# Optimization experiments

Hardware: AMD Instinct MI355X
Metric: run time of the kernel (lower is better)

Reference implementation:

```python
import jax, jax.numpy as jnp
import numpy as np

P = 16          # patch size
NH = 12         # num heads
DH = 64         # head dim
C = 768         # embed dim
DEPTH = 12
HID = 3072      # mlp hidden = 4*C
EPS = 1e-6


def _ln(x, g, b):
    m = x.mean(-1, keepdims=True)
    v = ((x - m) ** 2).mean(-1, keepdims=True)
    return (x - m) / jnp.sqrt(v + EPS) * g + b


def _rope_tables(seq_len, dim):
    inv_freq = 1.0 / (10000.0 ** (jnp.arange(0, dim, 2, dtype=jnp.float32) / dim))
    freqs = jnp.arange(seq_len, dtype=jnp.float32)[:, None] * inv_freq[None, :]  # [S, dim/2]
    emb = jnp.concatenate([freqs, freqs], axis=-1)  # [S, dim] (concat layout, as in source)
    return jnp.cos(emb), jnp.sin(emb)


def _apply_rope(q, k, cos, sin):
    def rot(t):  # interleaved rotate-half, exactly as torch source
        t1, t2 = t[..., ::2], t[..., 1::2]
        return jnp.stack([-t2, t1], axis=-1).reshape(t.shape)
    return q * cos + rot(q) * sin, k * cos + rot(k) * sin


def setup_inputs() -> dict:
    key = jax.random.key(0)
    ks = jax.random.split(key, 16)
    w = lambda k, shp: (jax.random.normal(k, shp, dtype=jnp.float32) * 0.02)
    inp = {
        "x": jax.random.normal(ks[0], (4, 6, 320, 320), dtype=jnp.float32),
        "conv_w": w(ks[1], (C, 3, P, P)),
        "conv_b": jnp.zeros((C,), jnp.float32),
        "ln1_g": jnp.ones((DEPTH, C), jnp.float32),
        "ln1_b": jnp.zeros((DEPTH, C), jnp.float32),
        "qkv_w": w(ks[2], (DEPTH, C, 3 * C)),
        "qkv_b": jnp.zeros((DEPTH, 3 * C), jnp.float32),
        "proj_w": w(ks[3], (DEPTH, C, C)),
        "proj_b": jnp.zeros((DEPTH, C), jnp.float32),
        "ln2_g": jnp.ones((DEPTH, C), jnp.float32),
        "ln2_b": jnp.zeros((DEPTH, C), jnp.float32),
        "fc1_w": w(ks[4], (DEPTH, C, HID)),
        "fc1_b": jnp.zeros((DEPTH, HID), jnp.float32),
        "fc2_w": w(ks[5], (DEPTH, HID, C)),
        "fc2_b": jnp.zeros((DEPTH, C), jnp.float32),
        "lnf_g": jnp.ones((C,), jnp.float32),
        "lnf_b": jnp.zeros((C,), jnp.float32),
    }
    return inp


def reference(x, conv_w, conv_b, ln1_g, ln1_b, qkv_w, qkv_b, proj_w, proj_b,
              ln2_g, ln2_b, fc1_w, fc1_b, fc2_w, fc2_b, lnf_g, lnf_b):
    B = x.shape[0]

    def embed(img):  # [B,3,H,W] -> [B, (H/P)*(W/P), C]
        y = jax.lax.conv_general_dilated(
            img, conv_w, window_strides=(P, P), padding="VALID",
            dimension_numbers=("NCHW", "OIHW", "NCHW")) + conv_b[None, :, None, None]
        b, c, hg, wg = y.shape
        return y.reshape(b, c, hg * wg).transpose(0, 2, 1)

    t = jnp.concatenate([embed(x[:, :3]), embed(x[:, 3:])], axis=1)  # [B,S,C], S=2*400=800
    S = t.shape[1]
    cos, sin = _rope_tables(S, DH)
    cos, sin = cos[None, None], sin[None, None]  # [1,1,S,DH]
    scale = DH ** -0.5

    def block(h, p):
        l1g, l1b, qw, qb, pw, pb, l2g, l2b, f1w, f1b, f2w, f2b = p
        y = _ln(h, l1g, l1b)
        qkv = (y @ qw + qb).reshape(B, S, 3, NH, DH).transpose(2, 0, 3, 1, 4)
        q, k, v = qkv[0], qkv[1], qkv[2]  # [B,NH,S,DH]
        q, k = _apply_rope(q, k, cos, sin)
        a = jax.nn.softmax(jnp.einsum("bhsd,bhtd->bhst", q, k) * scale, axis=-1)
        o = jnp.einsum("bhst,bhtd->bhsd", a, v).transpose(0, 2, 1, 3).reshape(B, S, C)
        h = h + (o @ pw + pb)
        y = _ln(h, l2g, l2b)
        h = h + (jax.nn.gelu(y @ f1w + f1b, approximate=False) @ f2w + f2b)
        return h, None

    params = (ln1_g, ln1_b, qkv_w, qkv_b, proj_w, proj_b,
              ln2_g, ln2_b, fc1_w, fc1_b, fc2_w, fc2_b)
    t, _ = jax.lax.scan(block, t, params)
    return _ln(t, lnf_g, lnf_b)
```

## Files before the change

kernel.cpp:

```cpp
#include <hip/hip_runtime.h>
#include <hip/hip_bf16.h>
#include <math.h>

#define S_LEN   800
#define SP_LEN  896
#define C_DIM   768
#define NHEAD   12
#define DHEAD   64
#define HID_DIM 3072
#define BATCH   4
#define NTOK    (BATCH * S_LEN)
#define DEPTH_N 12

using bf16x8 = __attribute__((ext_vector_type(8))) short;
using f32x4  = __attribute__((ext_vector_type(4))) float;

__device__ inline short f2bf(float x) {
    unsigned u = __builtin_bit_cast(unsigned, x);
    u += 0x7fff + ((u >> 16) & 1);
    return (short)(u >> 16);
}
__device__ inline float bf2f(short x) {
    unsigned u = ((unsigned)(unsigned short)x) << 16;
    return __builtin_bit_cast(float, u);
}

typedef const __attribute__((address_space(1))) void* gas_ptr;
typedef __attribute__((address_space(3))) void* las_ptr;
__device__ inline void async_copy16(const void* g, void* l) {
    __builtin_amdgcn_global_load_lds((gas_ptr)g, (las_ptr)l, 16, 0, 0);
}

__global__ __launch_bounds__(256)
void transpose_convert_kernel(const float* __restrict__ W, short* __restrict__ Wt,
                              int K, int N) {
    __shared__ float tile[32][33];
    int k0 = blockIdx.y * 32, n0 = blockIdx.x * 32;
    int tx = threadIdx.x & 31, ty = threadIdx.x >> 5;
#pragma unroll
    for (int i = ty; i < 32; i += 8)
        tile[i][tx] = W[(size_t)(k0 + i) * N + n0 + tx];
    __syncthreads();
#pragma unroll
    for (int i = ty; i < 32; i += 8)
        Wt[(size_t)(n0 + i) * K + k0 + tx] = f2bf(tile[tx][i]);
}

__global__ void convert_bf_kernel(const float* __restrict__ a, short* __restrict__ o, int n) {
    int i = blockIdx.x * 256 + threadIdx.x;
    if (i < n) o[i] = f2bf(a[i]);
}

__global__ void im2col_kernel(const float* __restrict__ x, short* __restrict__ A) {
    int idx = blockIdx.x * 256 + threadIdx.x;
    if (idx >= NTOK * 768) return;
    int kk = idx % 768;
    int s  = (idx / 768) % S_LEN;
    int b  = idx / (768 * S_LEN);
    int c  = kk / 256;
    int i  = (kk / 16) % 16;
    int j  = kk % 16;
    int half = s / 400, ss = s % 400;
    int hg = ss / 20, wg = ss % 20;
    int ch = half * 3 + c;
    A[idx] = f2bf(x[((size_t)(b * 6 + ch) * 320 + hg * 16 + i) * 320 + wg * 16 + j]);
}

template <int BN, bool GELU, bool RES, bool OBF>
__global__ __launch_bounds__(256)
void gemm_mfma(const short* __restrict__ A, const short* __restrict__ Bt,
               const float* __restrict__ bias, const float* __restrict__ res,
               void* __restrict__ Cout, int M, int N, int K) {
    constexpr int BM = 128, BK = 64;
    constexpr int TI = (BN == 128) ? 4 : 2;
    constexpr int TJ = 4;
    constexpr int ACALLS = BM * BK / (8 * 64);
    constexpr int BCALLS = BN * BK / (8 * 64);

    __shared__ __align__(16) short As[BM * BK];
    __shared__ __align__(16) short Bs[BN * BK];

    int tid = threadIdx.x;
    int w = tid >> 6, lane = tid & 63;
    int m0 = blockIdx.y * BM, n0 = blockIdx.x * BN;

    int wr = (BN == 128) ? (w >> 1) * 64 : w * 32;
    int wc = (BN == 128) ? (w & 1) * 64 : 0;

    f32x4 acc[TI][TJ];
#pragma unroll
    for (int i = 0; i < TI; ++i)
#pragma unroll
        for (int j = 0; j < TJ; ++j)
            acc[i][j] = (f32x4){0.f, 0.f, 0.f, 0.f};

    int lc = lane & 15, lq = lane >> 4;

    for (int k0 = 0; k0 < K; k0 += BK) {
#pragma unroll
        for (int j = w; j < ACALLS; j += 4) {
            int c = j * 64 + lane;
            int row = c >> 3, p = c & 7, q = p ^ (row & 7);
            async_copy16(A + (size_t)(m0 + row) * K + k0 + q * 8, As + j * 512);
        }
#pragma unroll
        for (int j = w; j < BCALLS; j += 4) {
            int c = j * 64 + lane;
            int row = c >> 3, p = c & 7, q = p ^ (row & 7);
            async_copy16(Bt + (size_t)(n0 + row) * K + k0 + q * 8, Bs + j * 512);
        }
        __syncthreads();

#pragma unroll
        for (int h = 0; h < 2; ++h) {
            bf16x8 afrag[TI], bfrag[TJ];
#pragma unroll
            for (int i = 0; i < TI; ++i) {
                int row = wr + i * 16 + lc;
                afrag[i] = *(const bf16x8*)(As + row * 64 + ((((h << 2) | lq)) ^ (row & 7)) * 8);
            }
#pragma unroll
            for (int j = 0; j < TJ; ++j) {
                int col = wc + j * 16 + lc;
                bfrag[j] = *(const bf16x8*)(Bs + col * 64 + ((((h << 2) | lq)) ^ (col & 7)) * 8);
            }
#pragma unroll
            for (int i = 0; i < TI; ++i)
#pragma unroll
                for (int j = 0; j < TJ; ++j)
                    acc[i][j] = __builtin_amdgcn_mfma_f32_16x16x32_bf16(
                        afrag[i], bfrag[j], acc[i][j], 0, 0, 0);
        }
        __syncthreads();
    }

    int rbase = lq * 4;
#pragma unroll
    for (int i = 0; i < TI; ++i)
#pragma unroll
        for (int j = 0; j < TJ; ++j)
#pragma unroll
            for (int r = 0; r < 4; ++r) {
                int m = m0 + wr + i * 16 + rbase + r;
                int n = n0 + wc + j * 16 + lc;
                float v = acc[i][j][r] + bias[n];
                if (RES) v += res[(size_t)m * N + n];
                if (GELU) v = 0.5f * v * (1.0f + erff(v * 0.70710678118654752f));
                if (OBF) ((short*)Cout)[(size_t)m * N + n] = f2bf(v);
                else     ((float*)Cout)[(size_t)m * N + n] = v;
            }
}

template <bool OBF>
__global__ __launch_bounds__(256)
void ln_kernel(const float* __restrict__ x, const float* __restrict__ g,
               const float* __restrict__ bta, void* __restrict__ yv) {
    int row = blockIdx.x;
    const float* xr = x + (size_t)row * C_DIM;
    int tid = threadIdx.x;

    float v0 = xr[tid], v1 = xr[tid + 256], v2 = xr[tid + 512];
    float s  = v0 + v1 + v2;
    float sq = v0 * v0 + v1 * v1 + v2 * v2;
#pragma unroll
    for (int off = 32; off; off >>= 1) {
        s  += __shfl_down(s, off);
        sq += __shfl_down(sq, off);
    }
    __shared__ float red1[4], red2[4];
    __shared__ float mean_s, rstd_s;
    int wv = tid / 64, lane = tid % 64;
    if (lane == 0) { red1[wv] = s; red2[wv] = sq; }
    __syncthreads();
    if (tid == 0) {
        float S1 = red1[0] + red1[1] + red1[2] + red1[3];
        float S2 = red2[0] + red2[1] + red2[2] + red2[3];
        float m = S1 / (float)C_DIM;
        float var = S2 / (float)C_DIM - m * m;
        mean_s = m;
        rstd_s = rsqrtf(var + 1e-6f);
    }
    __syncthreads();
    float m = mean_s, r = rstd_s;
    float o0 = (v0 - m) * r * g[tid]       + bta[tid];
    float o1 = (v1 - m) * r * g[tid + 256] + bta[tid + 256];
    float o2 = (v2 - m) * r * g[tid + 512] + bta[tid + 512];
    if (OBF) {
        short* yr = (short*)yv + (size_t)row * C_DIM;
        yr[tid] = f2bf(o0); yr[tid + 256] = f2bf(o1); yr[tid + 512] = f2bf(o2);
    } else {
        float* yr = (float*)yv + (size_t)row * C_DIM;
        yr[tid] = o0; yr[tid + 256] = o1; yr[tid + 512] = o2;
    }
}

__global__ __launch_bounds__(256)
void rope_qkv_kernel(const short* __restrict__ qkv, short* __restrict__ qb,
                     short* __restrict__ kb, short* __restrict__ vtb) {
    int st = blockIdx.x;
    int bh = blockIdx.y;
    int b = bh / NHEAD, h = bh % NHEAD;
    int s0 = st * 64;

    __shared__ __align__(16) short vlds[64][72];

    int tid = threadIdx.x;
    int sl = tid >> 2;
    int dc = (tid & 3) * 16;
    int s = s0 + sl;

    short qo[16], ko[16];
    if (s < S_LEN) {
        const short* base = qkv + ((size_t)(b * S_LEN + s)) * (3 * C_DIM) + h * DHEAD + dc;
        short qsh[16], ksh[16], vsh[16];
        *(bf16x8*)(qsh)     = *(const bf16x8*)(base);
        *(bf16x8*)(qsh + 8) = *(const bf16x8*)(base + 8);
        *(bf16x8*)(ksh)     = *(const bf16x8*)(base + C_DIM);
        *(bf16x8*)(ksh + 8) = *(const bf16x8*)(base + C_DIM + 8);
        *(bf16x8*)(vsh)     = *(const bf16x8*)(base + 2 * C_DIM);
        *(bf16x8*)(vsh + 8) = *(const bf16x8*)(base + 2 * C_DIM + 8);
        float qv[16], kv[16];
#pragma unroll
        for (int i = 0; i < 16; ++i) { qv[i] = bf2f(qsh[i]); kv[i] = bf2f(ksh[i]); }
#pragma unroll
        for (int i = 0; i < 16; ++i) {
            int d = dc + i;
            float ang = (float)s * exp2f(-(float)(d & 31) * 0.41524101186092029f);
            float c = cosf(ang), sn = sinf(ang);
            float sign = (i & 1) ? 1.0f : -1.0f;
            qo[i] = f2bf((qv[i] * c + sign * qv[i ^ 1] * sn) * 0.18033688011112042f);
            ko[i] = f2bf(kv[i] * c + sign * kv[i ^ 1] * sn);
        }
        *(bf16x8*)&vlds[sl][dc]     = *(bf16x8*)(vsh);
        *(bf16x8*)&vlds[sl][dc + 8] = *(bf16x8*)(vsh + 8);
    } else {
#pragma unroll
        for (int i = 0; i < 16; ++i) { qo[i] = 0; ko[i] = 0; vlds[sl][dc + i] = 0; }
    }
    {
        short* qd = qb + ((size_t)bh * SP_LEN + s) * DHEAD + dc;
        short* kd = kb + ((size_t)bh * SP_LEN + s) * DHEAD + dc;
        *(bf16x8*)(qd)     = *(bf16x8*)(qo);
        *(bf16x8*)(qd + 8) = *(bf16x8*)(qo + 8);
        *(bf16x8*)(kd)     = *(bf16x8*)(ko);
        *(bf16x8*)(kd + 8) = *(bf16x8*)(ko + 8);
    }
    __syncthreads();
    {
        int dr = tid >> 2, sc = (tid & 3) * 16;
        short vo[16];
#pragma unroll
        for (int i = 0; i < 16; ++i) vo[i] = vlds[sc + i][dr];
        short* vd = vtb + ((size_t)bh * DHEAD + dr) * SP_LEN + s0 + sc;
        *(bf16x8*)(vd)     = *(bf16x8*)(vo);
        *(bf16x8*)(vd + 8) = *(bf16x8*)(vo + 8);
    }
}

__global__ __launch_bounds__(256)
void attn_mfma_kernel(const short* __restrict__ qb, const short* __restrict__ kb,
                      const short* __restrict__ vtb, short* __restrict__ o) {
    int qt = blockIdx.x;
    int bh = blockIdx.y;
    int b = bh / NHEAD, h = bh % NHEAD;
    int m0 = qt * 64;

    __shared__ __align__(16) short Qs[64 * 64];
    __shared__ __align__(16) short Ks[128 * 64];
    __shared__ __align__(16) short Vts[64 * 128];
    __shared__ __align__(16) short Ps[64 * 136];

    int tid = threadIdx.x;
    int w = tid >> 6, lane = tid & 63;
    int lc = lane & 15, lq = lane >> 4;
    int kq = lq * 8;

    const short* qbase = qb + (size_t)bh * SP_LEN * DHEAD;
    const short* kbase = kb + (size_t)bh * SP_LEN * DHEAD;
    const short* vbase = vtb + (size_t)bh * DHEAD * SP_LEN;

    f32x4 oacc[4];
#pragma unroll
    for (int t = 0; t < 4; ++t) oacc[t] = (f32x4){0.f, 0.f, 0.f, 0.f};
    float mrow[4] = {-3.0e38f, -3.0e38f, -3.0e38f, -3.0e38f};
    float lrow[4] = {0.f, 0.f, 0.f, 0.f};

#pragma unroll
    for (int j = w; j < 8; j += 4) {
        int c = j * 64 + lane;
        int row = c >> 3, p = c & 7, q = p ^ (row & 7);
        async_copy16(qbase + (size_t)(m0 + row) * DHEAD + q * 8, Qs + j * 512);
    }

    for (int it = 0; it < 7; ++it) {
        int kt = it * 128;
#pragma unroll
        for (int j = w; j < 16; j += 4) {
            int c = j * 64 + lane;
            int row = c >> 3, p = c & 7, q = p ^ (row & 7);
            async_copy16(kbase + (size_t)(kt + row) * DHEAD + q * 8, Ks + j * 512);
        }
#pragma unroll
        for (int j = w; j < 16; j += 4) {
            int c = j * 64 + lane;
            int d = c >> 4, p = c & 15, sq = p ^ (d & 15);
            async_copy16(vbase + (size_t)d * SP_LEN + kt + sq * 8, Vts + j * 512);
        }
        __syncthreads();

        int nt = (it < 6) ? 8 : 2;

        int qrow = w * 16 + lc;
        bf16x8 aq0 = *(const bf16x8*)(Qs + qrow * 64 + ((lq) ^ (qrow & 7)) * 8);
        bf16x8 aq1 = *(const bf16x8*)(Qs + qrow * 64 + ((4 | lq) ^ (qrow & 7)) * 8);

        f32x4 sacc[8];
        for (int t = 0; t < nt; ++t) {
            int kr = t * 16 + lc;
            bf16x8 bk0 = *(const bf16x8*)(Ks + kr * 64 + ((lq) ^ (kr & 7)) * 8);
            bf16x8 bk1 = *(const bf16x8*)(Ks + kr * 64 + ((4 | lq) ^ (kr & 7)) * 8);
            f32x4 z = (f32x4){0.f, 0.f, 0.f, 0.f};
            z = __builtin_amdgcn_mfma_f32_16x16x32_bf16(aq0, bk0, z, 0, 0, 0);
            z = __builtin_amdgcn_mfma_f32_16x16x32_bf16(aq1, bk1, z, 0, 0, 0);
            sacc[t] = z;
        }

        float rmax[4];
#pragma unroll
        for (int r = 0; r < 4; ++r) {
            float m = sacc[0][r];
            for (int t = 1; t < nt; ++t) m = fmaxf(m, sacc[t][r]);
            rmax[r] = m;
        }
#pragma unroll
        for (int off = 1; off < 16; off <<= 1)
#pragma unroll
            for (int r = 0; r < 4; ++r)
                rmax[r] = fmaxf(rmax[r], __shfl_xor(rmax[r], off));

        float alpha[4], rsum[4] = {0.f, 0.f, 0.f, 0.f};
#pragma unroll
        for (int r = 0; r < 4; ++r) {
            float mnew = fmaxf(mrow[r], rmax[r]);
            alpha[r] = exp2f(mrow[r] - mnew);
            mrow[r] = mnew;
        }
        for (int t = 0; t < nt; ++t) {
#pragma unroll
            for (int r = 0; r < 4; ++r) {
                float p = exp2f(sacc[t][r] - mrow[r]);
                rsum[r] += p;
                Ps[(w * 16 + lq * 4 + r) * 136 + t * 16 + lc] = f2bf(p);
            }
        }
#pragma unroll
        for (int off = 1; off < 16; off <<= 1)
#pragma unroll
            for (int r = 0; r < 4; ++r)
                rsum[r] += __shfl_xor(rsum[r], off);
#pragma unroll
        for (int r = 0; r < 4; ++r) lrow[r] = lrow[r] * alpha[r] + rsum[r];
#pragma unroll
        for (int t = 0; t < 4; ++t)
#pragma unroll
            for (int r = 0; r < 4; ++r) oacc[t][r] *= alpha[r];

        int nk = (nt == 8) ? 4 : 1;
        for (int kstep = 0; kstep < nk; ++kstep) {
            bf16x8 ap = *(const bf16x8*)(Ps + (w * 16 + lc) * 136 + kstep * 32 + kq);
#pragma unroll
            for (int t = 0; t < 4; ++t) {
                int dr = t * 16 + lc;
                bf16x8 bv = *(const bf16x8*)(Vts + dr * 128 + ((((kstep << 2) | lq)) ^ (dr & 15)) * 8);
                oacc[t] = __builtin_amdgcn_mfma_f32_16x16x32_bf16(ap, bv, oacc[t], 0, 0, 0);
            }
        }
        __syncthreads();
    }

    float inv_l[4];
#pragma unroll
    for (int r = 0; r < 4; ++r) inv_l[r] = 1.0f / lrow[r];
#pragma unroll
    for (int t = 0; t < 4; ++t)
#pragma unroll
        for (int r = 0; r < 4; ++r) {
            int row = w * 16 + lq * 4 + r;
            int s = m0 + row;
            if (s < S_LEN) {
                int n = t * 16 + lc;
                o[((size_t)(b * S_LEN + s)) * C_DIM + h * DHEAD + n] = f2bf(oacc[t][r] * inv_l[r]);
            }
        }
}

extern "C" void kernel_launch(void* const* d_in, const int* in_sizes, int n_in,
                              void* d_out, int out_size, void* d_ws, size_t ws_size,
                              hipStream_t stream) {
    const float* x      = (const float*)d_in[0];
    const float* conv_w = (const float*)d_in[1];
    const float* conv_b = (const float*)d_in[2];
    const float* ln1_g  = (const float*)d_in[3];
    const float* ln1_b  = (const float*)d_in[4];
    const float* qkv_w  = (const float*)d_in[5];
    const float* qkv_b  = (const float*)d_in[6];
    const float* proj_w = (const float*)d_in[7];
    const float* proj_b = (const float*)d_in[8];
    const float* ln2_g  = (const float*)d_in[9];
    const float* ln2_b  = (const float*)d_in[10];
    const float* fc1_w  = (const float*)d_in[11];
    const float* fc1_b  = (const float*)d_in[12];
    const float* fc2_w  = (const float*)d_in[13];
    const float* fc2_b  = (const float*)d_in[14];
    const float* lnf_g  = (const float*)d_in[15];
    const float* lnf_b  = (const float*)d_in[16];

    const size_t NTC = (size_t)NTOK * C_DIM;
    const size_t HSD = (size_t)BATCH * NHEAD * SP_LEN * DHEAD;
    float* ws = (float*)d_ws;
    float* h       = ws;
    short* qkv_bf  = (short*)(h + NTC);
    short* qb      = qkv_bf + (size_t)NTOK * 3 * C_DIM;
    short* kb      = qb + HSD;
    short* vtb     = kb + HSD;
    short* y_bf    = vtb + HSD;
    short* big_bf  = y_bf + NTC;
    short* wbuf    = big_bf + (size_t)NTOK * HID_DIM;
    short* embed_wt = wbuf + (size_t)HID_DIM * C_DIM;

    convert_bf_kernel<<<(768 * 768 + 255) / 256, 256, 0, stream>>>(conv_w, embed_wt, 768 * 768);
    im2col_kernel<<<(NTOK * 768 + 255) / 256, 256, 0, stream>>>(x, big_bf);
    gemm_mfma<64, false, false, false><<<dim3(C_DIM / 64, NTOK / 128), 256, 0, stream>>>(
        big_bf, embed_wt, conv_b, nullptr, h, NTOK, C_DIM, C_DIM);

    for (int l = 0; l < DEPTH_N; ++l) {
        const float* l1g = ln1_g + (size_t)l * C_DIM;
        const float* l1b = ln1_b + (size_t)l * C_DIM;
        const float* qw  = qkv_w + (size_t)l * C_DIM * 3 * C_DIM;
        const float* qbs = qkv_b + (size_t)l * 3 * C_DIM;
        const float* pw  = proj_w + (size_t)l * C_DIM * C_DIM;
        const float* pb  = proj_b + (size_t)l * C_DIM;
        const float* l2g = ln2_g + (size_t)l * C_DIM;
        const float* l2b = ln2_b + (size_t)l * C_DIM;
        const float* f1w = fc1_w + (size_t)l * C_DIM * HID_DIM;
        const float* f1b = fc1_b + (size_t)l * HID_DIM;
        const float* f2w = fc2_w + (size_t)l * HID_DIM * C_DIM;
        const float* f2b = fc2_b + (size_t)l * C_DIM;

        ln_kernel<true><<<NTOK, 256, 0, stream>>>(h, l1g, l1b, y_bf);
        transpose_convert_kernel<<<dim3(3 * C_DIM / 32, C_DIM / 32), 256, 0, stream>>>(
            qw, wbuf, C_DIM, 3 * C_DIM);
        gemm_mfma<128, false, false, true><<<dim3(3 * C_DIM / 128, NTOK / 128), 256, 0, stream>>>(
            y_bf, wbuf, qbs, nullptr, qkv_bf, NTOK, 3 * C_DIM, C_DIM);

        rope_qkv_kernel<<<dim3(14, BATCH * NHEAD), 256, 0, stream>>>(qkv_bf, qb, kb, vtb);
        attn_mfma_kernel<<<dim3(13, BATCH * NHEAD), 256, 0, stream>>>(qb, kb, vtb, y_bf);

        transpose_convert_kernel<<<dim3(C_DIM / 32, C_DIM / 32), 256, 0, stream>>>(
            pw, wbuf, C_DIM, C_DIM);
        gemm_mfma<64, false, true, false><<<dim3(C_DIM / 64, NTOK / 128), 256, 0, stream>>>(
            y_bf, wbuf, pb, h, h, NTOK, C_DIM, C_DIM);

        ln_kernel<true><<<NTOK, 256, 0, stream>>>(h, l2g, l2b, y_bf);
        transpose_convert_kernel<<<dim3(HID_DIM / 32, C_DIM / 32), 256, 0, stream>>>(
            f1w, wbuf, C_DIM, HID_DIM);
        gemm_mfma<128, true, false, true><<<dim3(HID_DIM / 128, NTOK / 128), 256, 0, stream>>>(
            y_bf, wbuf, f1b, nullptr, big_bf, NTOK, HID_DIM, C_DIM);
        transpose_convert_kernel<<<dim3(C_DIM / 32, HID_DIM / 32), 256, 0, stream>>>(
            f2w, wbuf, HID_DIM, C_DIM);
        gemm_mfma<64, false, true, false><<<dim3(C_DIM / 64, NTOK / 128), 256, 0, stream>>>(
            big_bf, wbuf, f2b, h, h, NTOK, C_DIM, HID_DIM);
    }

    ln_kernel<false><<<NTOK, 256, 0, stream>>>(h, lnf_g, lnf_b, d_out);
}
```

Measured before the change: 2.803 ms.

## Batch weight transposes, remap GEMM blocks across XCDs, tune attention scheduling

Merges the four per-layer weight transpose/convert launches into one kernel that writes separate buffers, cutting launch count. GEMM workgroups are remapped so neighbouring tiles land on the same XCD for better L2 reuse. The attention and rope grids are reordered to put batch-head on x, Q fragments are loaded once instead of every iteration, and wave priority is raised around the MFMA loops. Workspace grows to hold all four transposed weights at once.

```diff
diff --git a/kernel.cpp b/kernel.cpp
--- a/kernel.cpp
+++ b/kernel.cpp
@@ -31,11 +31,23 @@
     __builtin_amdgcn_global_load_lds((gas_ptr)g, (las_ptr)l, 16, 0, 0);
 }
 
-__global__ __launch_bounds__(256)
-void transpose_convert_kernel(const float* __restrict__ W, short* __restrict__ Wt,
-                              int K, int N) {
+__device__ inline int xcd_remap(int bid, int nwg) {
+    int x = bid & 7, q = nwg >> 3, r = nwg & 7;
+    int base = (x < r) ? x * (q + 1) : r * (q + 1) + (x - r) * q;
+    return base + (bid >> 3);
+}
+
+struct TP4 {
+    const float *qw, *pw, *f1, *f2;
+    short *wq, *wp, *w1, *w2;
+};
+
+template <int K, int N>
+__device__ __forceinline__ void tc_tile(const float* __restrict__ W,
+                                        short* __restrict__ Wt, int t) {
     __shared__ float tile[32][33];
-    int k0 = blockIdx.y * 32, n0 = blockIdx.x * 32;
+    int nb = t % (N / 32), kb = t / (N / 32);
+    int k0 = kb * 32, n0 = nb * 32;
     int tx = threadIdx.x & 31, ty = threadIdx.x >> 5;
 #pragma unroll
     for (int i = ty; i < 32; i += 8)
@@ -44,6 +56,15 @@
 #pragma unroll
     for (int i = ty; i < 32; i += 8)
         Wt[(size_t)(n0 + i) * K + k0 + tx] = f2bf(tile[tx][i]);
+}
+
+__global__ __launch_bounds__(256)
+void transpose4_kernel(TP4 p) {
+    int t = blockIdx.x;
+    if (t < 1728)          tc_tile<768, 2304>(p.qw, p.wq, t);
+    else if (t < 2304)     tc_tile<768, 768>(p.pw, p.wp, t - 1728);
+    else if (t < 4608)     tc_tile<768, 3072>(p.f1, p.w1, t - 2304);
+    else                   tc_tile<3072, 768>(p.f2, p.w2, t - 4608);
 }
 
 __global__ void convert_bf_kernel(const float* __restrict__ a, short* __restrict__ o, int n) {
@@ -82,7 +103,11 @@
 
     int tid = threadIdx.x;
     int w = tid >> 6, lane = tid & 63;
-    int m0 = blockIdx.y * BM, n0 = blockIdx.x * BN;
+
+    int nwg = gridDim.x * gridDim.y;
+    int flat = xcd_remap(blockIdx.x + gridDim.x * blockIdx.y, nwg);
+    int bx = flat % gridDim.x, by = flat / gridDim.x;
+    int m0 = by * BM, n0 = bx * BN;
 
     int wr = (BN == 128) ? (w >> 1) * 64 : w * 32;
     int wc = (BN == 128) ? (w & 1) * 64 : 0;
@@ -197,8 +222,8 @@
 __global__ __launch_bounds__(256)
 void rope_qkv_kernel(const short* __restrict__ qkv, short* __restrict__ qb,
                      short* __restrict__ kb, short* __restrict__ vtb) {
-    int st = blockIdx.x;
-    int bh = blockIdx.y;
+    int bh = blockIdx.x;
+    int st = blockIdx.y;
     int b = bh / NHEAD, h = bh % NHEAD;
     int s0 = st * 64;
 
@@ -260,8 +285,8 @@
 __global__ __launch_bounds__(256)
 void attn_mfma_kernel(const short* __restrict__ qb, const short* __restrict__ kb,
                       const short* __restrict__ vtb, short* __restrict__ o) {
-    int qt = blockIdx.x;
-    int bh = blockIdx.y;
+    int bh = blockIdx.x;
+    int qt = blockIdx.y;
     int b = bh / NHEAD, h = bh % NHEAD;
     int m0 = qt * 64;
 
@@ -292,6 +317,8 @@
         async_copy16(qbase + (size_t)(m0 + row) * DHEAD + q * 8, Qs + j * 512);
     }
 
+    bf16x8 aq0, aq1;
+
     for (int it = 0; it < 7; ++it) {
         int kt = it * 128;
 #pragma unroll
@@ -310,11 +337,14 @@
 
         int nt = (it < 6) ? 8 : 2;
 
-        int qrow = w * 16 + lc;
-        bf16x8 aq0 = *(const bf16x8*)(Qs + qrow * 64 + ((lq) ^ (qrow & 7)) * 8);
-        bf16x8 aq1 = *(const bf16x8*)(Qs + qrow * 64 + ((4 | lq) ^ (qrow & 7)) * 8);
+        if (it == 0) {
+            int qrow = w * 16 + lc;
+            aq0 = *(const bf16x8*)(Qs + qrow * 64 + ((lq) ^ (qrow & 7)) * 8);
+            aq1 = *(const bf16x8*)(Qs + qrow * 64 + ((4 | lq) ^ (qrow & 7)) * 8);
+        }
 
         f32x4 sacc[8];
+        __builtin_amdgcn_s_setprio(1);
         for (int t = 0; t < nt; ++t) {
             int kr = t * 16 + lc;
             bf16x8 bk0 = *(const bf16x8*)(Ks + kr * 64 + ((lq) ^ (kr & 7)) * 8);
@@ -324,6 +354,7 @@
             z = __builtin_amdgcn_mfma_f32_16x16x32_bf16(aq1, bk1, z, 0, 0, 0);
             sacc[t] = z;
         }
+        __builtin_amdgcn_s_setprio(0);
 
         float rmax[4];
 #pragma unroll
@@ -366,6 +397,7 @@
             for (int r = 0; r < 4; ++r) oacc[t][r] *= alpha[r];
 
         int nk = (nt == 8) ? 4 : 1;
+        __builtin_amdgcn_s_setprio(1);
         for (int kstep = 0; kstep < nk; ++kstep) {
             bf16x8 ap = *(const bf16x8*)(Ps + (w * 16 + lc) * 136 + kstep * 32 + kq);
 #pragma unroll
@@ -375,6 +407,7 @@
                 oacc[t] = __builtin_amdgcn_mfma_f32_16x16x32_bf16(ap, bv, oacc[t], 0, 0, 0);
             }
         }
+        __builtin_amdgcn_s_setprio(0);
         __syncthreads();
     }
 
@@ -425,8 +458,11 @@
     short* vtb     = kb + HSD;
     short* y_bf    = vtb + HSD;
     short* big_bf  = y_bf + NTC;
-    short* wbuf    = big_bf + (size_t)NTOK * HID_DIM;
-    short* embed_wt = wbuf + (size_t)HID_DIM * C_DIM;
+    short* wq      = big_bf + (size_t)NTOK * HID_DIM;
+    short* wp      = wq + (size_t)3 * C_DIM * C_DIM;
+    short* w1      = wp + (size_t)C_DIM * C_DIM;
+    short* w2      = w1 + (size_t)C_DIM * HID_DIM;
+    short* embed_wt = w2 + (size_t)HID_DIM * C_DIM;
 
     convert_bf_kernel<<<(768 * 768 + 255) / 256, 256, 0, stream>>>(conv_w, embed_wt, 768 * 768);
     im2col_kernel<<<(NTOK * 768 + 255) / 256, 256, 0, stream>>>(x, big_bf);
@@ -447,29 +483,24 @@
         const float* f2w = fc2_w + (size_t)l * HID_DIM * C_DIM;
         const float* f2b = fc2_b + (size_t)l * C_DIM;
 
+        TP4 tp{qw, pw, f1w, f2w, wq, wp, w1, w2};
+        transpose4_kernel<<<6912, 256, 0, stream>>>(tp);
+
         ln_kernel<true><<<NTOK, 256, 0, stream>>>(h, l1g, l1b, y_bf);
-        transpose_convert_kernel<<<dim3(3 * C_DIM / 32, C_DIM / 32), 256, 0, stream>>>(
-            qw, wbuf, C_DIM, 3 * C_DIM);
         gemm_mfma<128, false, false, true><<<dim3(3 * C_DIM / 128, NTOK / 128), 256, 0, stream>>>(
-            y_bf, wbuf, qbs, nullptr, qkv_bf, NTOK, 3 * C_DIM, C_DIM);
-
-        rope_qkv_kernel<<<dim3(14, BATCH * NHEAD), 256, 0, stream>>>(qkv_bf, qb, kb, vtb);
-        attn_mfma_kernel<<<dim3(13, BATCH * NHEAD), 256, 0, stream>>>(qb, kb, vtb, y_bf);
-
-        transpose_convert_kernel<<<dim3(C_DIM / 32, C_DIM / 32), 256, 0, stream>>>(
-            pw, wbuf, C_DIM, C_DIM);
+            y_bf, wq, qbs, nullptr, qkv_bf, NTOK, 3 * C_DIM, C_DIM);
+
+        rope_qkv_kernel<<<dim3(BATCH * NHEAD, 14), 256, 0, stream>>>(qkv_bf, qb, kb, vtb);
+        attn_mfma_kernel<<<dim3(BATCH * NHEAD, 13), 256, 0, stream>>>(qb, kb, vtb, y_bf);
+
         gemm_mfma<64, false, true, false><<<dim3(C_DIM / 64, NTOK / 128), 256, 0, stream>>>(
-            y_bf, wbuf, pb, h, h, NTOK, C_DIM, C_DIM);
+            y_bf, wp, pb, h, h, NTOK, C_DIM, C_DIM);
 
         ln_kernel<true><<<NTOK, 256, 0, stream>>>(h, l2g, l2b, y_bf);
-        transpose_convert_kernel<<<dim3(HID_DIM / 32, C_DIM / 32), 256, 0, stream>>>(
-            f1w, wbuf, C_DIM, HID_DIM);
         gemm_mfma<128, true, false, true><<<dim3(HID_DIM / 128, NTOK / 128), 256, 0, stream>>>(
-            y_bf, wbuf, f1b, nullptr, big_bf, NTOK, HID_DIM, C_DIM);
-        transpose_convert_kernel<<<dim3(C_DIM / 32, HID_DIM / 32), 256, 0, stream>>>(
-            f2w, wbuf, HID_DIM, C_DIM);
+            y_bf, w1, f1b, nullptr, big_bf, NTOK, HID_DIM, C_DIM);
         gemm_mfma<64, false, true, false><<<dim3(C_DIM / 64, NTOK / 128), 256, 0, stream>>>(
-            big_bf, wbuf, f2b, h, h, NTOK, C_DIM, HID_DIM);
+            big_bf, w2, f2b, h, h, NTOK, C_DIM, HID_DIM);
     }
 
     ln_kernel<false><<<NTOK, 256, 0, stream>>>(h, lnf_g, lnf_b, d_out);
```

After: 2.645 ms. 1.06x faster.
